# Performance work log

Hardware: AMD Instinct MI355X
Metric: run time of the kernel (lower is better)

Reference implementation:

```python
import jax, jax.numpy as jnp
import numpy as np

B, L, S, H, E = 4, 2048, 2048, 8, 64

def setup_inputs() -> dict:
    key = jax.random.key(0)
    kq, kk, kv, kt, kd = jax.random.split(key, 5)
    return {
        "queries": jax.random.normal(kq, (B, L, H, E), dtype=jnp.float32),
        "keys": jax.random.normal(kk, (B, S, H, E), dtype=jnp.float32),
        "values": jax.random.normal(kv, (B, S, H, E), dtype=jnp.float32),
        "attn_mask": jnp.zeros((1,), dtype=bool),
        "tau": jax.random.uniform(kt, (B, 1), dtype=jnp.float32),
        "delta": jax.random.normal(kd, (B, 1), dtype=jnp.float32),
    }

def reference(queries, keys, values, attn_mask, tau, delta):
    # queries: [B,L,H,E], keys: [B,S,H,E], values: [B,S,H,D]
    Bq, Lq, Hq, Eq = queries.shape
    scale = 1.0 / jnp.sqrt(jnp.float32(Eq))
    scores = jnp.einsum('blhe,bshe->bhls', queries, keys)  # [B,H,L,S]
    scores = scores * tau.reshape(Bq, 1, 1, 1)             # per-batch tau scale
    scores = scores + delta.reshape(Bq, 1, 1, 1)           # per-batch delta bias
    A = jax.nn.softmax(scale * scores, axis=-1)            # dropout is identity at eval
    V = jnp.einsum('bhls,bshd->blhd', A, values)           # [B,L,H,D]
    return V
```

## Files before the change

kernel.cpp:

```cpp
#include <hip/hip_runtime.h>
#include <hip/hip_bf16.h>
#include <stdint.h>

#define LL 2048
#define SS 2048
#define HH 8
#define EE 64
#define RSG 512

typedef float v4f  __attribute__((ext_vector_type(4)));
typedef float v16f __attribute__((ext_vector_type(16)));
typedef short s4v  __attribute__((ext_vector_type(4)));
typedef short s8v  __attribute__((ext_vector_type(8)));

__device__ __forceinline__ short f2bf(float f) {
    unsigned u = __float_as_uint(f);
    u = (u + 0x7fffu + ((u >> 16) & 1u)) >> 16;
    return (short)u;
}

__device__ __forceinline__ s4v pack4bf(float a, float b, float c, float d) {
    float2 ab = make_float2(a, b), cd = make_float2(c, d);
    __hip_bfloat162 r0 = __float22bfloat162_rn(ab);
    __hip_bfloat162 r1 = __float22bfloat162_rn(cd);
    s4v r;
    __builtin_memcpy(&r, &r0, 4);
    __builtin_memcpy(((char*)&r) + 4, &r1, 4);
    return r;
}

__global__ __launch_bounds__(256)
void dsattn_prep(const float* __restrict__ kk, const float* __restrict__ vv,
                 short* __restrict__ kimg, short* __restrict__ vimg)
{
    __shared__ short T[32][520];
    const int t   = threadIdx.x;
    const int blk = blockIdx.x;
    const int isV = blk >> 7;
    const int b   = (blk & 127) >> 5;
    const int ts  = blk & 31;
    const float* src = (isV ? vv : kk) + ((size_t)b * SS + ts * 64) * RSG;
    short* dimg = isV ? vimg : kimg;

    #pragma unroll 1
    for (int half = 0; half < 2; ++half) {
        const float* hsrc = src + (size_t)(half * 32) * RSG;
        #pragma unroll
        for (int i = 0; i < 16; ++i) {
            int g = i * 256 + t;
            int row = g >> 7, c4 = (g & 127) << 2;
            v4f d = *(const v4f*)(hsrc + (size_t)row * RSG + c4);
            *(s4v*)&T[row][c4] = pack4bf(d[0], d[1], d[2], d[3]);
        }
        __syncthreads();

        if (!isV) {
            const int echunk = t >> 5, srow = t & 31;
            const s8v kv = *(const s8v*)&T[srow][0 * 64 + echunk * 8];
            (void)kv;
            #pragma unroll
            for (int h = 0; h < 8; ++h) {
                s8v ov = *(const s8v*)&T[srow][h * 64 + echunk * 8];
                short* dst = dimg + ((size_t)((b * 8 + h) * 32 + ts)) * 4096
                           + (echunk * 64 + half * 32 + srow) * 8;
                *(s8v*)dst = ov;
            }
        } else {
            const int c = (t >> 6) + half * 4, e = t & 63;
            const int sbase = 16 * (c >> 1) + 4 * (c & 1) - half * 32;
            #pragma unroll
            for (int h = 0; h < 8; ++h) {
                s8v ov;
                #pragma unroll
                for (int j = 0; j < 8; ++j) {
                    int s = sbase + 8 * (j >> 2) + (j & 3);
                    ov[j] = T[s][h * 64 + e];
                }
                short* dst = dimg + ((size_t)((b * 8 + h) * 32 + ts)) * 4096
                           + (c * 64 + e) * 8;
                *(s8v*)dst = ov;
            }
        }
        __syncthreads();
    }
}

__global__ __launch_bounds__(256, 2)
void dsattn_main(const float* __restrict__ q, const short* __restrict__ kimg,
                 const short* __restrict__ vimg, const float* __restrict__ tau,
                 float* __restrict__ out)
{
    __shared__ short KV[4][8192];

    const int t    = threadIdx.x;
    const int lane = t & 63;
    const int w    = t >> 6;
    const int l31  = lane & 31;
    const int hi   = lane >> 5;

    const int hw = blockIdx.x;
    const int wu = (hw & 7) * 64 + (hw >> 3);
    const int mt = wu & 15;
    const int h  = (wu >> 4) & 7;
    const int b  = wu >> 7;

    const float scf = 0.125f * 1.44269504088896f * tau[b];

    s8v qf[4];
    {
        const float* qb = q + ((size_t)b * LL + (size_t)mt * 128 + w * 32 + l31) * RSG
                            + h * EE + 8 * hi;
        #pragma unroll
        for (int ks = 0; ks < 4; ++ks) {
            v4f a0 = *(const v4f*)(qb + 16 * ks);
            v4f a1 = *(const v4f*)(qb + 16 * ks + 4);
            s4v p0 = pack4bf(a0[0] * scf, a0[1] * scf, a0[2] * scf, a0[3] * scf);
            s4v p1 = pack4bf(a1[0] * scf, a1[1] * scf, a1[2] * scf, a1[3] * scf);
            s8v f;
            #pragma unroll
            for (int j = 0; j < 4; ++j) { f[j] = p0[j]; f[4 + j] = p1[j]; }
            qf[ks] = f;
        }
    }

    const char* gsrc;
    {
        const size_t pan = (size_t)((b * 8 + h) * 32) * 8192;
        if (w < 2) gsrc = (const char*)kimg + pan + w * 4096 + lane * 16;
        else       gsrc = (const char*)vimg + pan + (w - 2) * 4096 + lane * 16;
    }

    #define STAGE(slot)                                                                   \
        {                                                                                 \
            _Pragma("unroll")                                                             \
            for (int j = 0; j < 4; ++j) {                                                 \
                __builtin_amdgcn_global_load_lds(                                         \
                    (const __attribute__((address_space(1))) unsigned*)(gsrc + j * 1024), \
                    (__attribute__((address_space(3))) unsigned*)&KV[slot][w * 2048 + j * 512], \
                    16, 0, 0);                                                            \
            }                                                                             \
            gsrc += 8192;                                                                 \
        }

    v16f oacc[2];
    #pragma unroll
    for (int mb = 0; mb < 2; ++mb)
        #pragma unroll
        for (int r = 0; r < 16; ++r) oacc[mb][r] = 0.0f;
    float rsum = 0.0f;

    const int rb = hi * 512 + l31 * 8;

    asm volatile("s_waitcnt vmcnt(0)" ::: "memory");
    __builtin_amdgcn_sched_barrier(0);
    STAGE(0);
    STAGE(1);
    STAGE(2);

    #pragma unroll 4
    for (int it = 0; it < 32; ++it) {
        const int p = it & 3;

        __builtin_amdgcn_sched_barrier(0);
        if (it <= 29)      asm volatile("s_waitcnt vmcnt(8)" ::: "memory");
        else if (it == 30) asm volatile("s_waitcnt vmcnt(4)" ::: "memory");
        else               asm volatile("s_waitcnt vmcnt(0)" ::: "memory");
        __builtin_amdgcn_s_barrier();
        __builtin_amdgcn_sched_barrier(0);

        if (it <= 28) STAGE((it + 3) & 3);

        const short* Kp = &KV[p][0];
        const short* Vp = &KV[p][4096];

        v16f st[2];
        #pragma unroll
        for (int mb = 0; mb < 2; ++mb) {
            v16f z;
            #pragma unroll
            for (int r = 0; r < 16; ++r) z[r] = 0.0f;
            #pragma unroll
            for (int ks = 0; ks < 4; ++ks) {
                s8v kf = *(const s8v*)&Kp[ks * 1024 + mb * 256 + rb];
                z = __builtin_amdgcn_mfma_f32_32x32x16_bf16(kf, qf[ks], z, 0, 0, 0);
            }
            st[mb] = z;
        }

        #pragma unroll
        for (int mb = 0; mb < 2; ++mb)
            #pragma unroll
            for (int r = 0; r < 16; ++r)
                st[mb][r] = __builtin_amdgcn_exp2f(st[mb][r]);
        float s0 = 0.f, s1 = 0.f;
        #pragma unroll
        for (int r = 0; r < 16; ++r) { s0 += st[0][r]; s1 += st[1][r]; }
        rsum += s0 + s1;

        s8v pf[4];
        #pragma unroll
        for (int tt = 0; tt < 4; ++tt) {
            int o = 8 * (tt & 1);
            const v16f& sv = st[tt >> 1];
            s4v lo = pack4bf(sv[o + 0], sv[o + 1], sv[o + 2], sv[o + 3]);
            s4v hs = pack4bf(sv[o + 4], sv[o + 5], sv[o + 6], sv[o + 7]);
            s8v f;
            #pragma unroll
            for (int j = 0; j < 4; ++j) { f[j] = lo[j]; f[4 + j] = hs[j]; }
            pf[tt] = f;
        }

        #pragma unroll
        for (int mb = 0; mb < 2; ++mb) {
            v16f acc = oacc[mb];
            #pragma unroll
            for (int ks = 0; ks < 4; ++ks) {
                s8v vf = *(const s8v*)&Vp[ks * 1024 + mb * 256 + rb];
                acc = __builtin_amdgcn_mfma_f32_32x32x16_bf16(vf, pf[ks], acc, 0, 0, 0);
            }
            oacc[mb] = acc;
        }
    }

    rsum += __shfl_xor(rsum, 32);
    const float inv = 1.0f / rsum;
    float* ob = out + ((size_t)b * LL + (size_t)mt * 128 + w * 32 + l31) * RSG + h * EE;
    #pragma unroll
    for (int mb = 0; mb < 2; ++mb)
        #pragma unroll
        for (int rq = 0; rq < 4; ++rq) {
            int e0 = 32 * mb + 8 * rq + 4 * hi;
            v4f o4 = { oacc[mb][4 * rq + 0] * inv, oacc[mb][4 * rq + 1] * inv,
                       oacc[mb][4 * rq + 2] * inv, oacc[mb][4 * rq + 3] * inv };
            *(v4f*)(ob + e0) = o4;
        }
}

extern "C" void kernel_launch(void* const* d_in, const int* in_sizes, int n_in,
                              void* d_out, int out_size, void* d_ws, size_t ws_size,
                              hipStream_t stream) {
    const float* q     = (const float*)d_in[0];
    const float* k     = (const float*)d_in[1];
    const float* v     = (const float*)d_in[2];
    const float* tau   = (const float*)d_in[4];
    float* out = (float*)d_out;

    short* kimg = (short*)d_ws;
    short* vimg = kimg + (size_t)4 * SS * RSG;

    dsattn_prep<<<dim3(256), dim3(256), 0, stream>>>(k, v, kimg, vimg);
    dsattn_main<<<dim3(512), dim3(256), 0, stream>>>(q, kimg, vimg, tau, out);
}
```

Before: 135.6 us.

## Load K fragments straight to registers and stage V in per-wave LDS

Replaces the block-shared 4-slot LDS ring, which needed a workgroup barrier every tile, with a per-wave scheme. Each wave now loads its K MFMA fragments directly from global memory into double-buffered registers, and streams V into its own two-slot LDS buffer with global_load_lds, so no s_barrier is needed. The goal is to remove barrier stalls and LDS traffic for K and to overlap the next tile's loads with the current tile's compute. In exchange, each wave fetches the full K and V tiles itself, which multiplies L2 traffic by the wave count and raises register pressure. The hand-placed vmcnt waits and the reuse of V slots also rely on subtle ordering.

Result: slower. 145.3 us (+7.1%).

```diff
diff --git a/kernel.cpp b/kernel.cpp
--- a/kernel.cpp
+++ b/kernel.cpp
@@ -56,8 +56,6 @@
 
         if (!isV) {
             const int echunk = t >> 5, srow = t & 31;
-            const s8v kv = *(const s8v*)&T[srow][0 * 64 + echunk * 8];
-            (void)kv;
             #pragma unroll
             for (int h = 0; h < 8; ++h) {
                 s8v ov = *(const s8v*)&T[srow][h * 64 + echunk * 8];
@@ -90,7 +88,7 @@
                  const short* __restrict__ vimg, const float* __restrict__ tau,
                  float* __restrict__ out)
 {
-    __shared__ short KV[4][8192];
+    __shared__ short VL[4][2][4096];
 
     const int t    = threadIdx.x;
     const int lane = t & 63;
@@ -123,23 +121,31 @@
         }
     }
 
-    const char* gsrc;
-    {
-        const size_t pan = (size_t)((b * 8 + h) * 32) * 8192;
-        if (w < 2) gsrc = (const char*)kimg + pan + w * 4096 + lane * 16;
-        else       gsrc = (const char*)vimg + pan + (w - 2) * 4096 + lane * 16;
-    }
-
-    #define STAGE(slot)                                                                   \
+    const size_t pan = (size_t)((b * 8 + h) * 32) * 8192;
+
+    const char* kgp = (const char*)kimg + pan + hi * 1024 + l31 * 16;
+
+    const char* gv = (const char*)vimg + pan + lane * 16;
+
+    #define STAGE_V(slot)                                                                 \
         {                                                                                 \
             _Pragma("unroll")                                                             \
-            for (int j = 0; j < 4; ++j) {                                                 \
+            for (int j = 0; j < 8; ++j) {                                                 \
                 __builtin_amdgcn_global_load_lds(                                         \
-                    (const __attribute__((address_space(1))) unsigned*)(gsrc + j * 1024), \
-                    (__attribute__((address_space(3))) unsigned*)&KV[slot][w * 2048 + j * 512], \
+                    (const __attribute__((address_space(1))) unsigned*)(gv + j * 1024),   \
+                    (__attribute__((address_space(3))) unsigned*)&VL[w][slot][j * 512],   \
                     16, 0, 0);                                                            \
             }                                                                             \
-            gsrc += 8192;                                                                 \
+            gv += 8192;                                                                   \
+        }
+
+    s8v kfA[8], kfB[8];
+    #define LOAD_K(dst, tile)                                                             \
+        {                                                                                 \
+            const char* kp_ = kgp + (size_t)(tile) * 8192;                                \
+            _Pragma("unroll")                                                             \
+            for (int f = 0; f < 8; ++f)                                                   \
+                dst[f] = *(const s8v*)(kp_ + (f >> 1) * 2048 + (f & 1) * 512);            \
         }
 
     v16f oacc[2];
@@ -153,73 +159,75 @@
 
     asm volatile("s_waitcnt vmcnt(0)" ::: "memory");
     __builtin_amdgcn_sched_barrier(0);
-    STAGE(0);
-    STAGE(1);
-    STAGE(2);
-
-    #pragma unroll 4
-    for (int it = 0; it < 32; ++it) {
-        const int p = it & 3;
-
-        __builtin_amdgcn_sched_barrier(0);
-        if (it <= 29)      asm volatile("s_waitcnt vmcnt(8)" ::: "memory");
-        else if (it == 30) asm volatile("s_waitcnt vmcnt(4)" ::: "memory");
-        else               asm volatile("s_waitcnt vmcnt(0)" ::: "memory");
-        __builtin_amdgcn_s_barrier();
-        __builtin_amdgcn_sched_barrier(0);
-
-        if (it <= 28) STAGE((it + 3) & 3);
-
-        const short* Kp = &KV[p][0];
-        const short* Vp = &KV[p][4096];
-
-        v16f st[2];
-        #pragma unroll
-        for (int mb = 0; mb < 2; ++mb) {
-            v16f z;
-            #pragma unroll
-            for (int r = 0; r < 16; ++r) z[r] = 0.0f;
-            #pragma unroll
-            for (int ks = 0; ks < 4; ++ks) {
-                s8v kf = *(const s8v*)&Kp[ks * 1024 + mb * 256 + rb];
-                z = __builtin_amdgcn_mfma_f32_32x32x16_bf16(kf, qf[ks], z, 0, 0, 0);
-            }
-            st[mb] = z;
-        }
-
-        #pragma unroll
-        for (int mb = 0; mb < 2; ++mb)
-            #pragma unroll
-            for (int r = 0; r < 16; ++r)
-                st[mb][r] = __builtin_amdgcn_exp2f(st[mb][r]);
-        float s0 = 0.f, s1 = 0.f;
-        #pragma unroll
-        for (int r = 0; r < 16; ++r) { s0 += st[0][r]; s1 += st[1][r]; }
-        rsum += s0 + s1;
-
-        s8v pf[4];
-        #pragma unroll
-        for (int tt = 0; tt < 4; ++tt) {
-            int o = 8 * (tt & 1);
-            const v16f& sv = st[tt >> 1];
-            s4v lo = pack4bf(sv[o + 0], sv[o + 1], sv[o + 2], sv[o + 3]);
-            s4v hs = pack4bf(sv[o + 4], sv[o + 5], sv[o + 6], sv[o + 7]);
-            s8v f;
-            #pragma unroll
-            for (int j = 0; j < 4; ++j) { f[j] = lo[j]; f[4 + j] = hs[j]; }
-            pf[tt] = f;
-        }
-
-        #pragma unroll
-        for (int mb = 0; mb < 2; ++mb) {
-            v16f acc = oacc[mb];
-            #pragma unroll
-            for (int ks = 0; ks < 4; ++ks) {
-                s8v vf = *(const s8v*)&Vp[ks * 1024 + mb * 256 + rb];
-                acc = __builtin_amdgcn_mfma_f32_32x32x16_bf16(vf, pf[ks], acc, 0, 0, 0);
-            }
-            oacc[mb] = acc;
-        }
+    STAGE_V(0);
+    LOAD_K(kfA, 0);
+    STAGE_V(1);
+
+    #define TILE_BODY(T, SLOT, KC, KN, DO_LDK, DO_STV)                                    \
+        {                                                                                 \
+            const short* Vp = &VL[w][SLOT][0];                                            \
+                                                      \
+            v16f st[2];                                                                   \
+            _Pragma("unroll")                                                             \
+            for (int mb = 0; mb < 2; ++mb) {                                              \
+                v16f z;                                                                   \
+                _Pragma("unroll")                                                         \
+                for (int r = 0; r < 16; ++r) z[r] = 0.0f;                                 \
+                _Pragma("unroll")                                                         \
+                for (int ks = 0; ks < 4; ++ks)                                            \
+                    z = __builtin_amdgcn_mfma_f32_32x32x16_bf16(KC[ks * 2 + mb], qf[ks],  \
+                                                                z, 0, 0, 0);              \
+                st[mb] = z;                                                               \
+            }                                                                             \
+            if (DO_LDK) LOAD_K(KN, (T) + 1);            \
+                                               \
+            _Pragma("unroll")                                                             \
+            for (int mb = 0; mb < 2; ++mb)                                                \
+                _Pragma("unroll")                                                         \
+                for (int r = 0; r < 16; ++r)                                              \
+                    st[mb][r] = __builtin_amdgcn_exp2f(st[mb][r]);                        \
+            float s0 = 0.f, s1 = 0.f;                                                     \
+            _Pragma("unroll")                                                             \
+            for (int r = 0; r < 16; ++r) { s0 += st[0][r]; s1 += st[1][r]; }              \
+            rsum += s0 + s1;                                                              \
+            s8v pf[4];                                                                    \
+            _Pragma("unroll")                                                             \
+            for (int tt = 0; tt < 4; ++tt) {                                              \
+                int o = 8 * (tt & 1);                                                     \
+                const v16f& sv = st[tt >> 1];                                             \
+                s4v lo = pack4bf(sv[o + 0], sv[o + 1], sv[o + 2], sv[o + 3]);             \
+                s4v hs = pack4bf(sv[o + 4], sv[o + 5], sv[o + 6], sv[o + 7]);             \
+                s8v f;                                                                    \
+                _Pragma("unroll")                                                         \
+                for (int j = 0; j < 4; ++j) { f[j] = lo[j]; f[4 + j] = hs[j]; }           \
+                pf[tt] = f;                                                               \
+            }                                                                             \
+                                        \
+            _Pragma("unroll")                                                             \
+            for (int mb = 0; mb < 2; ++mb) {                                              \
+                v16f acc = oacc[mb];                                                      \
+                _Pragma("unroll")                                                         \
+                for (int ks = 0; ks < 4; ++ks) {                                          \
+                    s8v vf = *(const s8v*)&Vp[ks * 1024 + mb * 256 + rb];                 \
+                    acc = __builtin_amdgcn_mfma_f32_32x32x16_bf16(vf, pf[ks], acc, 0, 0, 0); \
+                }                                                                         \
+                oacc[mb] = acc;                                                           \
+            }                                                                             \
+            if (DO_STV) STAGE_V(SLOT);                   \
+        }
+
+    #pragma unroll 1
+    for (int it = 0; it < 32; it += 2) {
+        __builtin_amdgcn_sched_barrier(0);
+        asm volatile("s_waitcnt vmcnt(16)" ::: "memory");
+        __builtin_amdgcn_sched_barrier(0);
+        TILE_BODY(it, 0, kfA, kfB,  true,  (it <= 29));
+
+        __builtin_amdgcn_sched_barrier(0);
+        if (it + 1 < 31) asm volatile("s_waitcnt vmcnt(16)" ::: "memory");
+        else             asm volatile("s_waitcnt vmcnt(8)"  ::: "memory");
+        __builtin_amdgcn_sched_barrier(0);
+        TILE_BODY(it + 1, 1, kfB, kfA,  (it <= 29),  (it <= 28));
     }
 
     rsum += __shfl_xor(rsum, 32);
```
